# Kernel tuning notes

Hardware: AMD Instinct MI355X
Metric: run time of the kernel (lower is better)

## Reference

```python
import jax, jax.numpy as jnp
import numpy as np

HEAD_SIZE = 64
EPS_GN = 1e-5 * 8 * 8  # GroupNorm eps = 1e-5 * head_size_divisor**2


def rwkv7_scan(w_raw, q, k, v, a, b):
    """RWKV-7 'wind backstepping' linear recurrence.
    Inputs [B,T,H,N]. Per step (matching the CUDA kernel):
      decay = exp(-exp(w_raw)); sa = S @ a; S = S*decay + sa b^T + v k^T; y = S @ q
    State S is [B,H,N_value,N_key]."""
    decay = jnp.exp(-jnp.exp(w_raw))
    B, T, H, N = q.shape
    xs = tuple(jnp.moveaxis(t, 1, 0) for t in (decay, q, k, v, a, b))  # [T,B,H,N]
    S0 = jnp.zeros((B, H, N, N), q.dtype)

    def step(S, inp):
        d, qt, kt, vt, at, bt = inp
        sa = jnp.einsum('bhij,bhj->bhi', S, at)
        S = S * d[:, :, None, :] + sa[..., None] * bt[:, :, None, :] + vt[..., None] * kt[:, :, None, :]
        y = jnp.einsum('bhij,bhj->bhi', S, qt)
        return S, y

    _, ys = jax.lax.scan(step, S0, xs)
    return jnp.moveaxis(ys, 0, 1)  # [B,T,H,N]


def setup_inputs() -> dict:
    key = jax.random.key(0)
    B, T, C, H, N = 4, 960, 2048, 32, 64
    Dw, Da, Dv, Dg = 96, 96, 64, 256
    ks = iter(jax.random.split(key, 40))

    def nrm(shape, s=0.02):
        return jax.random.normal(next(ks), shape, jnp.float32) * s

    def uni(shape):
        return jax.random.uniform(next(ks), shape, jnp.float32)

    return dict(
        x=nrm((B, T, C), 1.0),
        v_first=nrm((B, T, C), 1.0),
        x_r=uni((1, 1, C)), x_w=uni((1, 1, C)), x_k=uni((1, 1, C)),
        x_v=uni((1, 1, C)), x_a=uni((1, 1, C)), x_g=uni((1, 1, C)),
        w0=jnp.linspace(-7.0, -2.0, C, dtype=jnp.float32).reshape(1, 1, C) + 0.5,
        w1=nrm((C, Dw)), w2=nrm((Dw, C)),
        a0=nrm((1, 1, C)), a1=nrm((C, Da)), a2=nrm((Da, C)),
        v0=jnp.ones((1, 1, C), jnp.float32), v1=nrm((C, Dv)), v2=nrm((Dv, C)),
        g1=nrm((C, Dg)), g2=nrm((Dg, C)),
        k_k=jnp.full((1, 1, C), 0.85, jnp.float32),
        k_a=jnp.ones((1, 1, C), jnp.float32),
        r_k=nrm((H, N)),
        Wr=nrm((C, C)), Wk=nrm((C, C)), Wv=nrm((C, C)), Wo=nrm((C, C)),
        ln_w=jnp.ones((C,), jnp.float32), ln_b=jnp.zeros((C,), jnp.float32),
    )


def reference(x, v_first, x_r, x_w, x_k, x_v, x_a, x_g,
              w0, w1, w2, a0, a1, a2, v0, v1, v2, g1, g2,
              k_k, k_a, r_k, Wr, Wk, Wv, Wo, ln_w, ln_b):
    B, T, C = x.shape
    H = C // HEAD_SIZE
    # time_shift: ZeroPad2d((0,0,1,-1)) == shift right by 1 along T with zero at t=0
    x_prev = jnp.pad(x, ((0, 0), (1, 0), (0, 0)))[:, :T]
    xx = x_prev - x
    xr = x + xx * x_r; xw = x + xx * x_w; xk = x + xx * x_k
    xv = x + xx * x_v; xa = x + xx * x_a; xg = x + xx * x_g

    r = xr @ Wr.T
    w = -jax.nn.softplus(-(w0 + jnp.tanh(xw @ w1) @ w2)) - 0.5
    k = xk @ Wk.T
    v = xv @ Wv.T
    # layer_id != 0: residual-value mixing with first layer's value
    v = v + (v_first - v) * jax.nn.sigmoid(v0 + (xv @ v1) @ v2)
    a = jax.nn.sigmoid(a0 + (xa @ a1) @ a2)
    g = jax.nn.sigmoid(xg @ g1) @ g2

    kk = (k * k_k).reshape(B, T, H, HEAD_SIZE)
    kk = kk / jnp.maximum(jnp.linalg.norm(kk, axis=-1, keepdims=True), 1e-12)  # F.normalize
    kk = kk.reshape(B, T, C)
    k = k * (1 + (a - 1) * k_a)

    hs = lambda t: t.reshape(B, T, H, HEAD_SIZE)
    y = rwkv7_scan(hs(w), hs(r), hs(k), hs(v), hs(-kk), hs(kk * a)).reshape(B, T, C)

    # GroupNorm(H groups over C)
    yg = y.reshape(B, T, H, HEAD_SIZE)
    mu = yg.mean(-1, keepdims=True)
    var = yg.var(-1, keepdims=True)
    y = ((yg - mu) / jnp.sqrt(var + EPS_GN)).reshape(B, T, C) * ln_w + ln_b

    y = y + ((hs(r) * hs(k) * r_k).sum(-1, keepdims=True) * hs(v)).reshape(B, T, C)
    return (y * g) @ Wo.T
```

## Files before the change

### kernel.cpp

```cpp
#include <hip/hip_runtime.h>
#include <stdint.h>

#define BDIM 4
#define TDIM 960
#define CDIM 2048
#define HDIM 32
#define NDIM 64
#define BT   (BDIM*TDIM)

typedef unsigned short u16;
typedef __attribute__((ext_vector_type(8))) short short8;
typedef __attribute__((ext_vector_type(4))) float f32x4;

__device__ __forceinline__ float b2f(u16 u){
  union{unsigned int i; float f;}x; x.i=((unsigned int)u)<<16; return x.f;
}
__device__ __forceinline__ u16 f2b(float f){
  union{float f; unsigned int i;}x; x.f=f;
  unsigned int r = x.i + 0x7fffu + ((x.i>>16)&1u);
  return (u16)(r>>16);
}
__device__ __forceinline__ unsigned pk2(float lo, float hi){
  return (unsigned)f2b(lo) | ((unsigned)f2b(hi)<<16);
}
__device__ __forceinline__ void unpack8(uint4 p, float* o){
  o[0]=b2f((u16)(p.x&0xffff)); o[1]=b2f((u16)(p.x>>16));
  o[2]=b2f((u16)(p.y&0xffff)); o[3]=b2f((u16)(p.y>>16));
  o[4]=b2f((u16)(p.z&0xffff)); o[5]=b2f((u16)(p.z>>16));
  o[6]=b2f((u16)(p.w&0xffff)); o[7]=b2f((u16)(p.w>>16));
}
__device__ __forceinline__ uint4 pack8(const float* o){
  uint4 p;
  p.x = pk2(o[0],o[1]);
  p.y = pk2(o[2],o[3]);
  p.z = pk2(o[4],o[5]);
  p.w = pk2(o[6],o[7]);
  return p;
}
__device__ __forceinline__ void ld8f(const float* p, float* o){
  float4 a = *(const float4*)p;
  float4 b = *(const float4*)(p+4);
  o[0]=a.x;o[1]=a.y;o[2]=a.z;o[3]=a.w;o[4]=b.x;o[5]=b.y;o[6]=b.z;o[7]=b.w;
}
__device__ __forceinline__ float sigm(float x){ return 1.f/(1.f+expf(-x)); }
__device__ __forceinline__ void stc(float* p, float v){ *p = v; }
__device__ __forceinline__ void stc(u16* p, float v){ *p = f2b(v); }

__device__ __forceinline__ float row_red16(float x){
  x += __int_as_float(__builtin_amdgcn_update_dpp(0, __float_as_int(x), 0xB1,  0xF, 0xF, true));
  x += __int_as_float(__builtin_amdgcn_update_dpp(0, __float_as_int(x), 0x4E,  0xF, 0xF, true));
  x += __int_as_float(__builtin_amdgcn_update_dpp(0, __float_as_int(x), 0x141, 0xF, 0xF, true));
  x += __int_as_float(__builtin_amdgcn_update_dpp(0, __float_as_int(x), 0x140, 0xF, 0xF, true));
  return x;
}

__global__ __launch_bounds__(256) void cvt_kernel(const float* src, u16* dst){
  size_t i = ((size_t)blockIdx.x*256 + threadIdx.x)*8;
  float v[8]; ld8f(src+i, v);
  *(uint4*)(dst+i) = pack8(v);
}

struct TJob { const float* src; u16* dst; int R, Cs, DR, DC; };
struct TJobs8 { TJob j[8]; };

__global__ __launch_bounds__(256) void transpose_pad_kernel(TJobs8 jobs){
  TJob jb = jobs.j[blockIdx.z];
  int idx = blockIdx.x*256 + threadIdx.x;
  int total = jb.DR*jb.DC;
  if (idx >= total) return;
  int i = idx / jb.DC, k = idx % jb.DC;
  float v = 0.f;
  if (i < jb.Cs && k < jb.R) v = jb.src[(size_t)k*jb.Cs + i];
  jb.dst[idx] = f2b(v);
}

__global__ __launch_bounds__(256) void mix_kernel(
  const float* x,
  const float* cr, const float* cw, const float* ck,
  const float* cv, const float* ca, const float* cg,
  u16* mr, u16* mw, u16* mk, u16* mv, u16* ma, u16* mg)
{
  size_t tid = (size_t)blockIdx.x*256 + threadIdx.x;
  size_t base = tid*8;
  int c = (int)(base % CDIM);
  int row = (int)(base / CDIM);
  int t = row % TDIM;
  float xc[8], xp[8], xx[8], cf[8], o[8];
  ld8f(x+base, xc);
  if (t > 0) {
    ld8f(x+base-CDIM, xp);
  } else {
    for(int j=0;j<8;j++) xp[j]=0.f;
  }
  #pragma unroll
  for(int j=0;j<8;j++) xx[j]=xp[j]-xc[j];
#define DOMIX(CP, OP) do { ld8f(CP+c, cf); \
  _Pragma("unroll") for(int j=0;j<8;j++) o[j]=xc[j]+xx[j]*cf[j]; \
  *(uint4*)(OP+base)=pack8(o); } while(0)
  DOMIX(cr, mr); DOMIX(cw, mw); DOMIX(ck, mk);
  DOMIX(cv, mv); DOMIX(ca, ma); DOMIX(cg, mg);
#undef DOMIX
}

struct GemmJob {
  const u16* A; const u16* Bt; void* C;
  int nbm, nbn, K, lda, ldb, ldc;
};
struct GemmJobs { GemmJob j[4]; };

template<typename TC>
__global__ __launch_bounds__(256, 2) void gemm_bt_kernel(GemmJobs jobs){
  GemmJob jb = jobs.j[blockIdx.z];
  int bm = blockIdx.x % jb.nbm;
  int bn = blockIdx.x / jb.nbm;
  if (bn >= jb.nbn) return;
  __shared__ __attribute__((aligned(16))) u16 As[128*64];
  __shared__ __attribute__((aligned(16))) u16 Bs[128*64];
  int tid = threadIdx.x;
  int wave = tid>>6, lane = tid&63;
  int wr = wave>>1, wc = wave&1;
  f32x4 acc[4][4];
  #pragma unroll
  for(int i=0;i<4;i++)
    #pragma unroll
    for(int j=0;j<4;j++) acc[i][j] = (f32x4){0.f,0.f,0.f,0.f};
  const int rA0 = bm*128;
  const int rB0 = bn*128;
  int srow = (lane>>3);
  int scol = (lane&7)*8;
  for (int k0=0; k0<jb.K; k0+=64){
    #pragma unroll
    for (int it=0; it<4; ++it){
      int rr = wave*32 + it*8;
      const u16* gA = jb.A + (size_t)(rA0 + rr + srow)*jb.lda + (k0 + scol);
      __builtin_amdgcn_global_load_lds((const __attribute__((address_space(1))) void*)gA,
          (__attribute__((address_space(3))) void*)&As[rr*64], 16, 0, 0);
      const u16* gB = jb.Bt + (size_t)(rB0 + rr + srow)*jb.ldb + (k0 + scol);
      __builtin_amdgcn_global_load_lds((const __attribute__((address_space(1))) void*)gB,
          (__attribute__((address_space(3))) void*)&Bs[rr*64], 16, 0, 0);
    }
    __syncthreads();
    #pragma unroll
    for (int kc=0; kc<2; ++kc){
      short8 af[4], bfr[4];
      int ko = kc*32 + (lane>>4)*8;
      #pragma unroll
      for (int mi=0; mi<4; ++mi)
        af[mi] = *(const short8*)&As[(wr*64 + mi*16 + (lane&15))*64 + ko];
      #pragma unroll
      for (int ni=0; ni<4; ++ni)
        bfr[ni] = *(const short8*)&Bs[(wc*64 + ni*16 + (lane&15))*64 + ko];
      #pragma unroll
      for (int mi=0; mi<4; ++mi)
        #pragma unroll
        for (int ni=0; ni<4; ++ni)
          acc[mi][ni] = __builtin_amdgcn_mfma_f32_16x16x32_bf16(af[mi], bfr[ni], acc[mi][ni], 0, 0, 0);
    }
    __syncthreads();
  }
  TC* C = (TC*)jb.C;
  int cn = (lane&15);
  int rq = (lane>>4)*4;
  #pragma unroll
  for (int mi=0; mi<4; ++mi){
    #pragma unroll
    for (int ni=0; ni<4; ++ni){
      int col = rB0 + wc*64 + ni*16 + cn;
      int row = rA0 + wr*64 + mi*16 + rq;
      #pragma unroll
      for (int e=0; e<4; ++e)
        stc(&C[(size_t)(row+e)*jb.ldc + col], acc[mi][ni][e]);
    }
  }
}

__global__ __launch_bounds__(256) void act_kernel(u16* hw, u16* hg){
  int idx = blockIdx.x*256 + threadIdx.x;
  if (blockIdx.z==0){ if (idx < BT*128) hw[idx] = f2b(tanhf(b2f(hw[idx]))); }
  else              { if (idx < BT*256) hg[idx] = f2b(sigm(b2f(hg[idx]))); }
}

__global__ __launch_bounds__(256) void post_kernel(
  const u16* rbuf, const u16* kbuf, const u16* vraw, const float* vfirst,
  const u16* wl, const u16* al, const u16* vl,
  const float* w0, const float* a0, const float* v0,
  const float* kkc, const float* kac,
  float* dout, uint4* qki, uint4* abi, u16* vs)
{
  int row = blockIdx.x, tid = threadIdx.x;
  int c = tid*8;
  size_t base = (size_t)row*CDIM + c;
  float qf[8], kf[8], vr[8], vf[8], wlf[8], alf[8], vlf[8], w0f[8], a0f[8], v0f[8], kkf[8], kaf[8];
  unpack8(*(const uint4*)(rbuf+base), qf);
  unpack8(*(const uint4*)(kbuf+base), kf);
  unpack8(*(const uint4*)(vraw+base), vr);
  ld8f(vfirst+base, vf);
  unpack8(*(const uint4*)(wl+base), wlf);
  unpack8(*(const uint4*)(al+base), alf);
  unpack8(*(const uint4*)(vl+base), vlf);
  ld8f(w0+c, w0f);
  ld8f(a0+c, a0f);
  ld8f(v0+c, v0f);
  ld8f(kkc+c, kkf);
  ld8f(kac+c, kaf);
  float dv[8], av[8], vv[8], kkr[8], kfin[8], asv[8], bsv[8];
  float ssq = 0.f;
  #pragma unroll
  for (int j=0;j<8;j++){
    float wv = -log1pf(expf(-(w0f[j]+wlf[j]))) - 0.5f;
    dv[j]  = expf(-expf(wv));
    av[j]  = sigm(a0f[j]+alf[j]);
    vv[j]  = vr[j] + (vf[j]-vr[j])*sigm(v0f[j]+vlf[j]);
    kkr[j] = kf[j]*kkf[j];
    ssq   += kkr[j]*kkr[j];
    kfin[j]= kf[j]*(1.f + (av[j]-1.f)*kaf[j]);
  }
  ssq += __shfl_xor(ssq,1); ssq += __shfl_xor(ssq,2); ssq += __shfl_xor(ssq,4);
  float inv = 1.f/fmaxf(sqrtf(ssq), 1e-12f);
  #pragma unroll
  for (int j=0;j<8;j++){ float kkn = kkr[j]*inv; asv[j] = -kkn; bsv[j] = kkn*av[j]; }
  *(float4*)(dout+base)   = make_float4(dv[0],dv[1],dv[2],dv[3]);
  *(float4*)(dout+base+4) = make_float4(dv[4],dv[5],dv[6],dv[7]);
  uint4* qke = (uint4*)((char*)qki + (size_t)row*8192 + (size_t)c*4);
  qke[0] = make_uint4(pk2(qf[0],qf[1]), pk2(kfin[0],kfin[1]), pk2(qf[2],qf[3]), pk2(kfin[2],kfin[3]));
  qke[1] = make_uint4(pk2(qf[4],qf[5]), pk2(kfin[4],kfin[5]), pk2(qf[6],qf[7]), pk2(kfin[6],kfin[7]));
  uint4* abe = (uint4*)((char*)abi + (size_t)row*8192 + (size_t)c*4);
  abe[0] = make_uint4(pk2(asv[0],asv[1]), pk2(bsv[0],bsv[1]), pk2(asv[2],asv[3]), pk2(bsv[2],bsv[3]));
  abe[1] = make_uint4(pk2(asv[4],asv[5]), pk2(bsv[4],bsv[5]), pk2(asv[6],asv[7]), pk2(bsv[6],bsv[7]));
  *(uint4*)(vs+base) = pack8(vv);
}

__global__ __launch_bounds__(256, 2) void scan_kernel(
  const float* __restrict__ decayp, const uint4* __restrict__ qki,
  const uint4* __restrict__ abi, const u16* __restrict__ vs,
  float* __restrict__ yb)
{
  int blk = blockIdx.x;
  int b    = blk >> 7;
  int h    = (blk >> 2) & 31;
  int qtr  = blk & 3;
  int tid  = threadIdx.x;
  int jg   = tid & 15;
  int ii   = tid >> 4;
  int row  = qtr*16 + ii;

  const char* dP = (const char*)decayp + (size_t)b*TDIM*8192 + h*256 + jg*16;
  const char* qP = (const char*)qki    + (size_t)b*TDIM*8192 + h*256 + jg*16;
  const char* aP = (const char*)abi    + (size_t)b*TDIM*8192 + h*256 + jg*16;
  const char* vP = (const char*)vs     + (size_t)b*TDIM*4096 + h*128 + row*2;

  float S0=0.f, S1=0.f, S2=0.f, S3=0.f;

  struct SR { f32x4 d; uint4 qk; uint4 ab; u16 v; };
  auto ld = [&](int t)->SR{
    SR r; size_t o = (size_t)t*8192;
    r.d  = *(const f32x4*)(dP + o);
    r.qk = *(const uint4*)(qP + o);
    r.ab = *(const uint4*)(aP + o);
    r.v  = *(const u16*)(vP + (size_t)t*4096);
    return r;
  };
  auto dostep = [&](const SR& r)->float{
    float a0=b2f((u16)(r.ab.x&0xffff)), a1=b2f((u16)(r.ab.x>>16));
    float a2=b2f((u16)(r.ab.z&0xffff)), a3=b2f((u16)(r.ab.z>>16));
    float sap = (S0*a0 + S1*a1) + (S2*a2 + S3*a3);
    sap = row_red16(sap);
    float c0=b2f((u16)(r.ab.y&0xffff)), c1=b2f((u16)(r.ab.y>>16));
    float c2=b2f((u16)(r.ab.w&0xffff)), c3=b2f((u16)(r.ab.w>>16));
    float k0=b2f((u16)(r.qk.y&0xffff)), k1=b2f((u16)(r.qk.y>>16));
    float k2=b2f((u16)(r.qk.w&0xffff)), k3=b2f((u16)(r.qk.w>>16));
    float vi=b2f(r.v);
    S0 = S0*r.d[0] + sap*c0 + vi*k0;
    S1 = S1*r.d[1] + sap*c1 + vi*k1;
    S2 = S2*r.d[2] + sap*c2 + vi*k2;
    S3 = S3*r.d[3] + sap*c3 + vi*k3;
    return (S0*b2f((u16)(r.qk.x&0xffff)) + S1*b2f((u16)(r.qk.x>>16)))
         + (S2*b2f((u16)(r.qk.z&0xffff)) + S3*b2f((u16)(r.qk.z>>16)));
  };

  SR A0=ld(0), A1=ld(1), A2=ld(2), A3=ld(3), A4=ld(4), A5=ld(5), A6=ld(6), A7=ld(7);
  for (int g=0; g<120; ++g){
    int tn = g*8 + 8;
    float yp[8];
#define STEPR(AR, S_) { yp[S_] = dostep(AR); int t_ = tn + (S_); \
    AR = ld(t_ < TDIM ? t_ : TDIM-1); }
    STEPR(A0,0) STEPR(A1,1) __builtin_amdgcn_sched_barrier(0);
    STEPR(A2,2) STEPR(A3,3) __builtin_amdgcn_sched_barrier(0);
    STEPR(A4,4) STEPR(A5,5) __builtin_amdgcn_sched_barrier(0);
    STEPR(A6,6) STEPR(A7,7) __builtin_amdgcn_sched_barrier(0);
#undef STEPR
    #pragma unroll
    for (int s=0; s<8; ++s) yp[s] = row_red16(yp[s]);
    if (jg < 8){
      float out = 0.f;
      #pragma unroll
      for (int s=0; s<8; ++s) if (jg==s) out = yp[s];
      yb[(size_t)b*TDIM*CDIM + (size_t)(g*8+jg)*CDIM + h*NDIM + row] = out;
    }
  }
}

__global__ __launch_bounds__(256) void final_kernel(
  const float* yb, const uint4* qki, const u16* vs,
  const float* rk, const float* lnw, const float* lnb, const u16* gl, u16* yg)
{
  int row = blockIdx.x, tid = threadIdx.x;
  int c = tid*8;
  size_t base = (size_t)row*CDIM + c;
  float y[8], rf[8], kf[8], vf[8], rkf[8], lw[8], lb[8], gf[8];
  ld8f(yb+base, y);
  const uint4* qke = (const uint4*)((const char*)qki + (size_t)row*8192 + (size_t)c*4);
  uint4 e0 = qke[0], e1 = qke[1];
  rf[0]=b2f((u16)(e0.x&0xffff)); rf[1]=b2f((u16)(e0.x>>16));
  rf[2]=b2f((u16)(e0.z&0xffff)); rf[3]=b2f((u16)(e0.z>>16));
  rf[4]=b2f((u16)(e1.x&0xffff)); rf[5]=b2f((u16)(e1.x>>16));
  rf[6]=b2f((u16)(e1.z&0xffff)); rf[7]=b2f((u16)(e1.z>>16));
  kf[0]=b2f((u16)(e0.y&0xffff)); kf[1]=b2f((u16)(e0.y>>16));
  kf[2]=b2f((u16)(e0.w&0xffff)); kf[3]=b2f((u16)(e0.w>>16));
  kf[4]=b2f((u16)(e1.y&0xffff)); kf[5]=b2f((u16)(e1.y>>16));
  kf[6]=b2f((u16)(e1.w&0xffff)); kf[7]=b2f((u16)(e1.w>>16));
  unpack8(*(const uint4*)(vs+base), vf);
  ld8f(rk+c,  rkf);
  ld8f(lnw+c, lw);
  ld8f(lnb+c, lb);
  unpack8(*(const uint4*)(gl+base), gf);
  float sy=0.f, syy=0.f, coef=0.f;
  #pragma unroll
  for (int j=0;j<8;j++){ sy+=y[j]; syy+=y[j]*y[j]; coef += rf[j]*kf[j]*rkf[j]; }
  sy  += __shfl_xor(sy,1);  sy  += __shfl_xor(sy,2);  sy  += __shfl_xor(sy,4);
  syy += __shfl_xor(syy,1); syy += __shfl_xor(syy,2); syy += __shfl_xor(syy,4);
  coef+= __shfl_xor(coef,1);coef+= __shfl_xor(coef,2);coef+= __shfl_xor(coef,4);
  float mu  = sy*(1.f/64.f);
  float var = syy*(1.f/64.f) - mu*mu;
  float rs  = rsqrtf(var + 6.4e-4f);
  float o[8];
  #pragma unroll
  for (int j=0;j<8;j++)
    o[j] = (((y[j]-mu)*rs)*lw[j] + lb[j] + coef*vf[j]) * gf[j];
  *(uint4*)(yg+base) = pack8(o);
}

extern "C" void kernel_launch(void* const* d_in, const int* in_sizes, int n_in,
                              void* d_out, int out_size, void* d_ws, size_t ws_size,
                              hipStream_t stream)
{
  const float* x      = (const float*)d_in[0];
  const float* vfirst = (const float*)d_in[1];
  const float* c_r = (const float*)d_in[2];
  const float* c_w = (const float*)d_in[3];
  const float* c_k = (const float*)d_in[4];
  const float* c_v = (const float*)d_in[5];
  const float* c_a = (const float*)d_in[6];
  const float* c_g = (const float*)d_in[7];
  const float* w0i = (const float*)d_in[8];
  const float* w1i = (const float*)d_in[9];
  const float* w2i = (const float*)d_in[10];
  const float* a0i = (const float*)d_in[11];
  const float* a1i = (const float*)d_in[12];
  const float* a2i = (const float*)d_in[13];
  const float* v0i = (const float*)d_in[14];
  const float* v1i = (const float*)d_in[15];
  const float* v2i = (const float*)d_in[16];
  const float* g1i = (const float*)d_in[17];
  const float* g2i = (const float*)d_in[18];
  const float* kki = (const float*)d_in[19];
  const float* kai = (const float*)d_in[20];
  const float* rki = (const float*)d_in[21];
  const float* Wr  = (const float*)d_in[22];
  const float* Wk  = (const float*)d_in[23];
  const float* Wv  = (const float*)d_in[24];
  const float* Wo  = (const float*)d_in[25];
  const float* lnw = (const float*)d_in[26];
  const float* lnb = (const float*)d_in[27];

  char* ws = (char*)d_ws;
  const size_t S2 = (size_t)BT*CDIM*2;
  u16* MIXR = (u16*)(ws + 0*S2);
  u16* MIXW = (u16*)(ws + 1*S2);
  u16* MIXK = (u16*)(ws + 2*S2);
  u16* MIXV = (u16*)(ws + 3*S2);
  u16* MIXA = (u16*)(ws + 4*S2);
  u16* MIXG = (u16*)(ws + 5*S2);
  u16* RBUF = (u16*)(ws + 6*S2);
  u16* KBUF = (u16*)(ws + 7*S2);
  u16* VRAW = (u16*)(ws + 8*S2);
  char* WB = ws + 9*S2;
  u16* WSLOT = (u16*)WB;
  char* WT = WB + 8388608;
  u16* W1T = (u16*)(WT + 0);
  u16* A1T = (u16*)(WT + 524288);
  u16* V1T = (u16*)(WT + 1048576);
  u16* G1T = (u16*)(WT + 1572864);
  u16* W2T = (u16*)(WT + 2621440);
  u16* A2T = (u16*)(WT + 3145728);
  u16* V2T = (u16*)(WT + 3670016);
  u16* G2T = (u16*)(WT + 4194304);
  char* HB = WT + 5242880;
  u16* HW = (u16*)(HB + 0);
  u16* HA = (u16*)(HB + 983040);
  u16* HV = (u16*)(HB + 1966080);
  u16* HG = (u16*)(HB + 2949120);
  char* L2 = HB + 4915200;
  u16* WL = (u16*)(L2 + 0*S2);
  u16* AL = (u16*)(L2 + 1*S2);
  u16* VL = (u16*)(L2 + 2*S2);
  u16* GL = (u16*)(L2 + 3*S2);
  float* WDEC = (float*)(ws + 0*S2);
  uint4* QKI  = (uint4*)(ws + 2*S2);
  uint4* ABI  = (uint4*)(ws + 4*S2);
  u16*   VS6  = (u16*)(ws + 6*S2);
  float* YBUF = (float*)(L2 + 0*S2);
  u16* YG = (u16*)(L2 + 2*S2);
  (void)in_sizes; (void)n_in; (void)out_size; (void)ws_size;

  TJobs8 tj;
  tj.j[0] = (TJob){w1i, W1T, 2048,  96, 128, 2048};
  tj.j[1] = (TJob){a1i, A1T, 2048,  96, 128, 2048};
  tj.j[2] = (TJob){v1i, V1T, 2048,  64, 128, 2048};
  tj.j[3] = (TJob){g1i, G1T, 2048, 256, 256, 2048};
  tj.j[4] = (TJob){w2i, W2T,   96, 2048, 2048, 128};
  tj.j[5] = (TJob){a2i, A2T,   96, 2048, 2048, 128};
  tj.j[6] = (TJob){v2i, V2T,   64, 2048, 2048, 128};
  tj.j[7] = (TJob){g2i, G2T,  256, 2048, 2048, 256};
  transpose_pad_kernel<<<dim3(2048,1,8), 256, 0, stream>>>(tj);

  mix_kernel<<<dim3(BT*CDIM/8/256), 256, 0, stream>>>(
      x, c_r, c_w, c_k, c_v, c_a, c_g, MIXR, MIXW, MIXK, MIXV, MIXA, MIXG);

  {
    GemmJobs gj;
    cvt_kernel<<<dim3(2048), 256, 0, stream>>>(Wr, WSLOT);
    gj.j[0] = (GemmJob){MIXR, WSLOT, RBUF, 30, 16, 2048, 2048, 2048, 2048};
    gj.j[1] = gj.j[0]; gj.j[2] = gj.j[0]; gj.j[3] = gj.j[0];
    gemm_bt_kernel<u16><<<dim3(480,1,1), 256, 0, stream>>>(gj);
    cvt_kernel<<<dim3(2048), 256, 0, stream>>>(Wk, WSLOT);
    gj.j[0] = (GemmJob){MIXK, WSLOT, KBUF, 30, 16, 2048, 2048, 2048, 2048};
    gemm_bt_kernel<u16><<<dim3(480,1,1), 256, 0, stream>>>(gj);
    cvt_kernel<<<dim3(2048), 256, 0, stream>>>(Wv, WSLOT);
    gj.j[0] = (GemmJob){MIXV, WSLOT, VRAW, 30, 16, 2048, 2048, 2048, 2048};
    gemm_bt_kernel<u16><<<dim3(480,1,1), 256, 0, stream>>>(gj);
  }

  GemmJobs lj1;
  lj1.j[0] = (GemmJob){MIXW, W1T, HW, 30, 1, 2048, 2048, 2048, 128};
  lj1.j[1] = (GemmJob){MIXA, A1T, HA, 30, 1, 2048, 2048, 2048, 128};
  lj1.j[2] = (GemmJob){MIXV, V1T, HV, 30, 1, 2048, 2048, 2048, 128};
  lj1.j[3] = (GemmJob){MIXG, G1T, HG, 30, 2, 2048, 2048, 2048, 256};
  gemm_bt_kernel<u16><<<dim3(60,1,4), 256, 0, stream>>>(lj1);

  act_kernel<<<dim3(3840,1,2), 256, 0, stream>>>(HW, HG);

  GemmJobs lj2;
  lj2.j[0] = (GemmJob){HW, W2T, WL, 30, 16, 128, 128, 128, 2048};
  lj2.j[1] = (GemmJob){HA, A2T, AL, 30, 16, 128, 128, 128, 2048};
  lj2.j[2] = (GemmJob){HV, V2T, VL, 30, 16, 128, 128, 128, 2048};
  lj2.j[3] = (GemmJob){HG, G2T, GL, 30, 16, 256, 256, 256, 2048};
  gemm_bt_kernel<u16><<<dim3(480,1,4), 256, 0, stream>>>(lj2);

  post_kernel<<<dim3(BT), 256, 0, stream>>>(
      RBUF, KBUF, VRAW, vfirst, WL, AL, VL, w0i, a0i, v0i, kki, kai,
      WDEC, QKI, ABI, VS6);

  scan_kernel<<<dim3(512), 256, 0, stream>>>(
      WDEC, QKI, ABI, VS6, YBUF);

  final_kernel<<<dim3(BT), 256, 0, stream>>>(
      YBUF, QKI, VS6, rki, lnw, lnb, GL, YG);

  cvt_kernel<<<dim3(2048), 256, 0, stream>>>(Wo, WSLOT);
  GemmJobs oj;
  oj.j[0] = (GemmJob){YG, WSLOT, d_out, 30, 16, 2048, 2048, 2048, 2048};
  oj.j[1] = oj.j[0]; oj.j[2] = oj.j[0]; oj.j[3] = oj.j[0];
  gemm_bt_kernel<float><<<dim3(480,1,1), 256, 0, stream>>>(oj);
}
```

Baseline: 823.3 us.

## Split scan state across 32 lanes per row with 1024 blocks

```diff
diff --git a/kernel.cpp b/kernel.cpp
--- a/kernel.cpp
+++ b/kernel.cpp
@@ -52,6 +52,9 @@
   x += __int_as_float(__builtin_amdgcn_update_dpp(0, __float_as_int(x), 0x141, 0xF, 0xF, true));
   x += __int_as_float(__builtin_amdgcn_update_dpp(0, __float_as_int(x), 0x140, 0xF, 0xF, true));
   return x;
+}
+__device__ __forceinline__ float xor16(float x){
+  return __int_as_float(__builtin_amdgcn_ds_swizzle(__float_as_int(x), 0x401F));
 }
 
 __global__ __launch_bounds__(256) void cvt_kernel(const float* src, u16* dst){
@@ -230,52 +233,47 @@
   *(uint4*)(vs+base) = pack8(vv);
 }
 
-__global__ __launch_bounds__(256, 2) void scan_kernel(
-  const float* __restrict__ decayp, const uint4* __restrict__ qki,
-  const uint4* __restrict__ abi, const u16* __restrict__ vs,
+__global__ __launch_bounds__(256, 4) void scan_kernel(
+  const float* __restrict__ decayp, const uint2* __restrict__ qki,
+  const uint2* __restrict__ abi, const u16* __restrict__ vs,
   float* __restrict__ yb)
 {
   int blk = blockIdx.x;
-  int b    = blk >> 7;
-  int h    = (blk >> 2) & 31;
-  int qtr  = blk & 3;
-  int tid  = threadIdx.x;
-  int jg   = tid & 15;
-  int ii   = tid >> 4;
-  int row  = qtr*16 + ii;
-
-  const char* dP = (const char*)decayp + (size_t)b*TDIM*8192 + h*256 + jg*16;
-  const char* qP = (const char*)qki    + (size_t)b*TDIM*8192 + h*256 + jg*16;
-  const char* aP = (const char*)abi    + (size_t)b*TDIM*8192 + h*256 + jg*16;
+  int b   = blk >> 8;
+  int h   = (blk >> 3) & 31;
+  int oct = blk & 7;
+  int tid = threadIdx.x;
+  int jg  = tid & 31;
+  int ii  = tid >> 5;
+  int row = oct*8 + ii;
+
+  const char* dP = (const char*)decayp + (size_t)b*TDIM*8192 + h*256 + jg*8;
+  const char* qP = (const char*)qki    + (size_t)b*TDIM*8192 + h*256 + jg*8;
+  const char* aP = (const char*)abi    + (size_t)b*TDIM*8192 + h*256 + jg*8;
   const char* vP = (const char*)vs     + (size_t)b*TDIM*4096 + h*128 + row*2;
 
-  float S0=0.f, S1=0.f, S2=0.f, S3=0.f;
-
-  struct SR { f32x4 d; uint4 qk; uint4 ab; u16 v; };
+  float Sx=0.f, Sy=0.f;
+
+  struct SR { float2 d; uint2 qk; uint2 ab; u16 v; };
   auto ld = [&](int t)->SR{
     SR r; size_t o = (size_t)t*8192;
-    r.d  = *(const f32x4*)(dP + o);
-    r.qk = *(const uint4*)(qP + o);
-    r.ab = *(const uint4*)(aP + o);
+    r.d  = *(const float2*)(dP + o);
+    r.qk = *(const uint2*)(qP + o);
+    r.ab = *(const uint2*)(aP + o);
     r.v  = *(const u16*)(vP + (size_t)t*4096);
     return r;
   };
   auto dostep = [&](const SR& r)->float{
-    float a0=b2f((u16)(r.ab.x&0xffff)), a1=b2f((u16)(r.ab.x>>16));
-    float a2=b2f((u16)(r.ab.z&0xffff)), a3=b2f((u16)(r.ab.z>>16));
-    float sap = (S0*a0 + S1*a1) + (S2*a2 + S3*a3);
+    float aLo=b2f((u16)(r.ab.x&0xffff)), aHi=b2f((u16)(r.ab.x>>16));
+    float sap = Sx*aLo + Sy*aHi;
     sap = row_red16(sap);
-    float c0=b2f((u16)(r.ab.y&0xffff)), c1=b2f((u16)(r.ab.y>>16));
-    float c2=b2f((u16)(r.ab.w&0xffff)), c3=b2f((u16)(r.ab.w>>16));
-    float k0=b2f((u16)(r.qk.y&0xffff)), k1=b2f((u16)(r.qk.y>>16));
-    float k2=b2f((u16)(r.qk.w&0xffff)), k3=b2f((u16)(r.qk.w>>16));
-    float vi=b2f(r.v);
-    S0 = S0*r.d[0] + sap*c0 + vi*k0;
-    S1 = S1*r.d[1] + sap*c1 + vi*k1;
-    S2 = S2*r.d[2] + sap*c2 + vi*k2;
-    S3 = S3*r.d[3] + sap*c3 + vi*k3;
-    return (S0*b2f((u16)(r.qk.x&0xffff)) + S1*b2f((u16)(r.qk.x>>16)))
-         + (S2*b2f((u16)(r.qk.z&0xffff)) + S3*b2f((u16)(r.qk.z>>16)));
+    sap += xor16(sap);
+    float bLo=b2f((u16)(r.ab.y&0xffff)), bHi=b2f((u16)(r.ab.y>>16));
+    float kLo=b2f((u16)(r.qk.y&0xffff)), kHi=b2f((u16)(r.qk.y>>16));
+    float vi =b2f(r.v);
+    Sx = Sx*r.d.x + sap*bLo + vi*kLo;
+    Sy = Sy*r.d.y + sap*bHi + vi*kHi;
+    return Sx*b2f((u16)(r.qk.x&0xffff)) + Sy*b2f((u16)(r.qk.x>>16));
   };
 
   SR A0=ld(0), A1=ld(1), A2=ld(2), A3=ld(3), A4=ld(4), A5=ld(5), A6=ld(6), A7=ld(7);
@@ -290,7 +288,10 @@
     STEPR(A6,6) STEPR(A7,7) __builtin_amdgcn_sched_barrier(0);
 #undef STEPR
     #pragma unroll
-    for (int s=0; s<8; ++s) yp[s] = row_red16(yp[s]);
+    for (int s=0; s<8; ++s){
+      yp[s] = row_red16(yp[s]);
+      yp[s] += xor16(yp[s]);
+    }
     if (jg < 8){
       float out = 0.f;
       #pragma unroll
@@ -461,8 +462,8 @@
       RBUF, KBUF, VRAW, vfirst, WL, AL, VL, w0i, a0i, v0i, kki, kai,
       WDEC, QKI, ABI, VS6);
 
-  scan_kernel<<<dim3(512), 256, 0, stream>>>(
-      WDEC, QKI, ABI, VS6, YBUF);
+  scan_kernel<<<dim3(1024), 256, 0, stream>>>(
+      WDEC, (const uint2*)QKI, (const uint2*)ABI, VS6, YBUF);
 
   final_kernel<<<dim3(BT), 256, 0, stream>>>(
       YBUF, QKI, VS6, rki, lnw, lnb, GL, YG);
```

New measurement: 986.8 us. +19.9%, slower.

## Store scan operands as fp32 planar arrays and precompute r·k coefficient in post

Applied to the files above, without the earlier changes.

```diff
diff --git a/kernel.cpp b/kernel.cpp
--- a/kernel.cpp
+++ b/kernel.cpp
@@ -11,6 +11,7 @@
 typedef unsigned short u16;
 typedef __attribute__((ext_vector_type(8))) short short8;
 typedef __attribute__((ext_vector_type(4))) float f32x4;
+typedef __attribute__((ext_vector_type(2))) float f32x2;
 
 __device__ __forceinline__ float b2f(u16 u){
   union{unsigned int i; float f;}x; x.i=((unsigned int)u)<<16; return x.f;
@@ -45,6 +46,8 @@
 __device__ __forceinline__ float sigm(float x){ return 1.f/(1.f+expf(-x)); }
 __device__ __forceinline__ void stc(float* p, float v){ *p = v; }
 __device__ __forceinline__ void stc(u16* p, float v){ *p = f2b(v); }
+__device__ __forceinline__ f32x2 lo2(f32x4 v){ return __builtin_shufflevector(v, v, 0, 1); }
+__device__ __forceinline__ f32x2 hi2(f32x4 v){ return __builtin_shufflevector(v, v, 2, 3); }
 
 __device__ __forceinline__ float row_red16(float x){
   x += __int_as_float(__builtin_amdgcn_update_dpp(0, __float_as_int(x), 0xB1,  0xF, 0xF, true));
@@ -184,13 +187,14 @@
   const u16* rbuf, const u16* kbuf, const u16* vraw, const float* vfirst,
   const u16* wl, const u16* al, const u16* vl,
   const float* w0, const float* a0, const float* v0,
-  const float* kkc, const float* kac,
-  float* dout, uint4* qki, uint4* abi, u16* vs)
+  const float* kkc, const float* kac, const float* rki,
+  float* dout, float* af, float* bf, float* kflo, float* kfhi,
+  u16* vs, float* coefp)
 {
   int row = blockIdx.x, tid = threadIdx.x;
   int c = tid*8;
   size_t base = (size_t)row*CDIM + c;
-  float qf[8], kf[8], vr[8], vf[8], wlf[8], alf[8], vlf[8], w0f[8], a0f[8], v0f[8], kkf[8], kaf[8];
+  float qf[8], kf[8], vr[8], vf[8], wlf[8], alf[8], vlf[8], w0f[8], a0f[8], v0f[8], kkf[8], kaf[8], rkf[8];
   unpack8(*(const uint4*)(rbuf+base), qf);
   unpack8(*(const uint4*)(kbuf+base), kf);
   unpack8(*(const uint4*)(vraw+base), vr);
@@ -203,6 +207,7 @@
   ld8f(v0+c, v0f);
   ld8f(kkc+c, kkf);
   ld8f(kac+c, kaf);
+  ld8f(rki+c, rkf);
   float dv[8], av[8], vv[8], kkr[8], kfin[8], asv[8], bsv[8];
   float ssq = 0.f;
   #pragma unroll
@@ -217,23 +222,35 @@
   }
   ssq += __shfl_xor(ssq,1); ssq += __shfl_xor(ssq,2); ssq += __shfl_xor(ssq,4);
   float inv = 1.f/fmaxf(sqrtf(ssq), 1e-12f);
-  #pragma unroll
-  for (int j=0;j<8;j++){ float kkn = kkr[j]*inv; asv[j] = -kkn; bsv[j] = kkn*av[j]; }
+  float coef = 0.f;
+  #pragma unroll
+  for (int j=0;j<8;j++){
+    float kkn = kkr[j]*inv; asv[j] = -kkn; bsv[j] = kkn*av[j];
+    coef += qf[j]*kfin[j]*rkf[j];
+  }
+  coef += __shfl_xor(coef,1); coef += __shfl_xor(coef,2); coef += __shfl_xor(coef,4);
+  __syncthreads();
   *(float4*)(dout+base)   = make_float4(dv[0],dv[1],dv[2],dv[3]);
   *(float4*)(dout+base+4) = make_float4(dv[4],dv[5],dv[6],dv[7]);
-  uint4* qke = (uint4*)((char*)qki + (size_t)row*8192 + (size_t)c*4);
-  qke[0] = make_uint4(pk2(qf[0],qf[1]), pk2(kfin[0],kfin[1]), pk2(qf[2],qf[3]), pk2(kfin[2],kfin[3]));
-  qke[1] = make_uint4(pk2(qf[4],qf[5]), pk2(kfin[4],kfin[5]), pk2(qf[6],qf[7]), pk2(kfin[6],kfin[7]));
-  uint4* abe = (uint4*)((char*)abi + (size_t)row*8192 + (size_t)c*4);
-  abe[0] = make_uint4(pk2(asv[0],asv[1]), pk2(bsv[0],bsv[1]), pk2(asv[2],asv[3]), pk2(bsv[2],bsv[3]));
-  abe[1] = make_uint4(pk2(asv[4],asv[5]), pk2(bsv[4],bsv[5]), pk2(asv[6],asv[7]), pk2(bsv[6],bsv[7]));
+  float* afp = af + base;
+  *(float4*)(afp)   = make_float4(asv[0],asv[1],asv[2],asv[3]);
+  *(float4*)(afp+4) = make_float4(asv[4],asv[5],asv[6],asv[7]);
+  float* bfp = bf + base;
+  *(float4*)(bfp)   = make_float4(bsv[0],bsv[1],bsv[2],bsv[3]);
+  *(float4*)(bfp+4) = make_float4(bsv[4],bsv[5],bsv[6],bsv[7]);
+  float* kfp = (c < 1024) ? (kflo + (size_t)row*1024 + c)
+                          : (kfhi + (size_t)row*1024 + (c-1024));
+  *(float4*)(kfp)   = make_float4(kfin[0],kfin[1],kfin[2],kfin[3]);
+  *(float4*)(kfp+4) = make_float4(kfin[4],kfin[5],kfin[6],kfin[7]);
   *(uint4*)(vs+base) = pack8(vv);
+  if ((tid&7)==0) coefp[(size_t)row*32 + (tid>>3)] = coef;
 }
 
 __global__ __launch_bounds__(256, 2) void scan_kernel(
-  const float* __restrict__ decayp, const uint4* __restrict__ qki,
-  const uint4* __restrict__ abi, const u16* __restrict__ vs,
-  float* __restrict__ yb)
+  const float* __restrict__ decayp, const u16* __restrict__ qb,
+  const float* __restrict__ kflo, const float* __restrict__ kfhi,
+  const float* __restrict__ af, const float* __restrict__ bf,
+  const u16* __restrict__ vs, float* __restrict__ yb)
 {
   int blk = blockIdx.x;
   int b    = blk >> 7;
@@ -244,38 +261,43 @@
   int ii   = tid >> 4;
   int row  = qtr*16 + ii;
 
-  const char* dP = (const char*)decayp + (size_t)b*TDIM*8192 + h*256 + jg*16;
-  const char* qP = (const char*)qki    + (size_t)b*TDIM*8192 + h*256 + jg*16;
-  const char* aP = (const char*)abi    + (size_t)b*TDIM*8192 + h*256 + jg*16;
-  const char* vP = (const char*)vs     + (size_t)b*TDIM*4096 + h*128 + row*2;
-
-  float S0=0.f, S1=0.f, S2=0.f, S3=0.f;
-
-  struct SR { f32x4 d; uint4 qk; uint4 ab; u16 v; };
+  size_t co4 = (size_t)(h*256 + jg*16);
+  const char* dP = (const char*)decayp + (size_t)b*TDIM*8192 + co4;
+  const char* aP = (const char*)af     + (size_t)b*TDIM*8192 + co4;
+  const char* bP = (const char*)bf     + (size_t)b*TDIM*8192 + co4;
+  const char* kP = (h < 16)
+      ? ((const char*)kflo + (size_t)b*TDIM*4096 + (size_t)(h*256 + jg*16))
+      : ((const char*)kfhi + (size_t)b*TDIM*4096 + (size_t)((h-16)*256 + jg*16));
+  const char* qP = (const char*)qb + (size_t)b*TDIM*4096 + (size_t)(h*128 + jg*8);
+  const char* vP = (const char*)vs + (size_t)b*TDIM*4096 + (size_t)(h*128 + row*2);
+
+  f32x2 Sa = (f32x2){0.f,0.f}, Sb = (f32x2){0.f,0.f};
+
+  struct SR { f32x4 d, k, a, b; uint2 q; u16 v; };
   auto ld = [&](int t)->SR{
-    SR r; size_t o = (size_t)t*8192;
-    r.d  = *(const f32x4*)(dP + o);
-    r.qk = *(const uint4*)(qP + o);
-    r.ab = *(const uint4*)(aP + o);
-    r.v  = *(const u16*)(vP + (size_t)t*4096);
+    SR r;
+    size_t o8 = (size_t)t*8192, o4 = (size_t)t*4096;
+    r.d = *(const f32x4*)(dP + o8);
+    r.a = *(const f32x4*)(aP + o8);
+    r.b = *(const f32x4*)(bP + o8);
+    r.k = *(const f32x4*)(kP + o4);
+    r.q = *(const uint2*)(qP + o4);
+    r.v = *(const u16*)(vP + o4);
     return r;
   };
   auto dostep = [&](const SR& r)->float{
-    float a0=b2f((u16)(r.ab.x&0xffff)), a1=b2f((u16)(r.ab.x>>16));
-    float a2=b2f((u16)(r.ab.z&0xffff)), a3=b2f((u16)(r.ab.z>>16));
-    float sap = (S0*a0 + S1*a1) + (S2*a2 + S3*a3);
+    f32x2 t = Sa*lo2(r.a) + Sb*hi2(r.a);
+    float sap = t[0] + t[1];
     sap = row_red16(sap);
-    float c0=b2f((u16)(r.ab.y&0xffff)), c1=b2f((u16)(r.ab.y>>16));
-    float c2=b2f((u16)(r.ab.w&0xffff)), c3=b2f((u16)(r.ab.w>>16));
-    float k0=b2f((u16)(r.qk.y&0xffff)), k1=b2f((u16)(r.qk.y>>16));
-    float k2=b2f((u16)(r.qk.w&0xffff)), k3=b2f((u16)(r.qk.w>>16));
-    float vi=b2f(r.v);
-    S0 = S0*r.d[0] + sap*c0 + vi*k0;
-    S1 = S1*r.d[1] + sap*c1 + vi*k1;
-    S2 = S2*r.d[2] + sap*c2 + vi*k2;
-    S3 = S3*r.d[3] + sap*c3 + vi*k3;
-    return (S0*b2f((u16)(r.qk.x&0xffff)) + S1*b2f((u16)(r.qk.x>>16)))
-         + (S2*b2f((u16)(r.qk.z&0xffff)) + S3*b2f((u16)(r.qk.z>>16)));
+    float vi = b2f(r.v);
+    f32x2 s2 = (f32x2){sap,sap};
+    f32x2 v2 = (f32x2){vi,vi};
+    Sa = Sa*lo2(r.d) + s2*lo2(r.b) + v2*lo2(r.k);
+    Sb = Sb*hi2(r.d) + s2*hi2(r.b) + v2*hi2(r.k);
+    f32x2 q01 = (f32x2){b2f((u16)(r.q.x&0xffff)), b2f((u16)(r.q.x>>16))};
+    f32x2 q23 = (f32x2){b2f((u16)(r.q.y&0xffff)), b2f((u16)(r.q.y>>16))};
+    f32x2 u = Sa*q01 + Sb*q23;
+    return u[0] + u[1];
   };
 
   SR A0=ld(0), A1=ld(1), A2=ld(2), A3=ld(3), A4=ld(4), A5=ld(5), A6=ld(6), A7=ld(7);
@@ -301,35 +323,24 @@
 }
 
 __global__ __launch_bounds__(256) void final_kernel(
-  const float* yb, const uint4* qki, const u16* vs,
-  const float* rk, const float* lnw, const float* lnb, const u16* gl, u16* yg)
+  const float* yb, const u16* vs, const float* coefp,
+  const float* lnw, const float* lnb, const u16* gl, u16* yg)
 {
   int row = blockIdx.x, tid = threadIdx.x;
   int c = tid*8;
   size_t base = (size_t)row*CDIM + c;
-  float y[8], rf[8], kf[8], vf[8], rkf[8], lw[8], lb[8], gf[8];
+  float y[8], vf[8], lw[8], lb[8], gf[8];
   ld8f(yb+base, y);
-  const uint4* qke = (const uint4*)((const char*)qki + (size_t)row*8192 + (size_t)c*4);
-  uint4 e0 = qke[0], e1 = qke[1];
-  rf[0]=b2f((u16)(e0.x&0xffff)); rf[1]=b2f((u16)(e0.x>>16));
-  rf[2]=b2f((u16)(e0.z&0xffff)); rf[3]=b2f((u16)(e0.z>>16));
-  rf[4]=b2f((u16)(e1.x&0xffff)); rf[5]=b2f((u16)(e1.x>>16));
-  rf[6]=b2f((u16)(e1.z&0xffff)); rf[7]=b2f((u16)(e1.z>>16));
-  kf[0]=b2f((u16)(e0.y&0xffff)); kf[1]=b2f((u16)(e0.y>>16));
-  kf[2]=b2f((u16)(e0.w&0xffff)); kf[3]=b2f((u16)(e0.w>>16));
-  kf[4]=b2f((u16)(e1.y&0xffff)); kf[5]=b2f((u16)(e1.y>>16));
-  kf[6]=b2f((u16)(e1.w&0xffff)); kf[7]=b2f((u16)(e1.w>>16));
   unpack8(*(const uint4*)(vs+base), vf);
-  ld8f(rk+c,  rkf);
   ld8f(lnw+c, lw);
   ld8f(lnb+c, lb);
   unpack8(*(const uint4*)(gl+base), gf);
-  float sy=0.f, syy=0.f, coef=0.f;
-  #pragma unroll
-  for (int j=0;j<8;j++){ sy+=y[j]; syy+=y[j]*y[j]; coef += rf[j]*kf[j]*rkf[j]; }
+  float coef = coefp[(size_t)row*32 + (tid>>3)];
+  float sy=0.f, syy=0.f;
+  #pragma unroll
+  for (int j=0;j<8;j++){ sy+=y[j]; syy+=y[j]*y[j]; }
   sy  += __shfl_xor(sy,1);  sy  += __shfl_xor(sy,2);  sy  += __shfl_xor(sy,4);
   syy += __shfl_xor(syy,1); syy += __shfl_xor(syy,2); syy += __shfl_xor(syy,4);
-  coef+= __shfl_xor(coef,1);coef+= __shfl_xor(coef,2);coef+= __shfl_xor(coef,4);
   float mu  = sy*(1.f/64.f);
   float var = syy*(1.f/64.f) - mu*mu;
   float rs  = rsqrtf(var + 6.4e-4f);
@@ -406,9 +417,12 @@
   u16* VL = (u16*)(L2 + 2*S2);
   u16* GL = (u16*)(L2 + 3*S2);
   float* WDEC = (float*)(ws + 0*S2);
-  uint4* QKI  = (uint4*)(ws + 2*S2);
-  uint4* ABI  = (uint4*)(ws + 4*S2);
-  u16*   VS6  = (u16*)(ws + 6*S2);
+  float* AF   = (float*)(ws + 2*S2);
+  float* BF   = (float*)(ws + 4*S2);
+  float* KFLO = (float*)(ws + 7*S2);
+  float* KFHI = (float*)(ws + 8*S2);
+  u16*   VSW  = (u16*)(WB);
+  float* COEF = (float*)(WB + 15728640);
   float* YBUF = (float*)(L2 + 0*S2);
   u16* YG = (u16*)(L2 + 2*S2);
   (void)in_sizes; (void)n_in; (void)out_size; (void)ws_size;
@@ -458,14 +472,14 @@
   gemm_bt_kernel<u16><<<dim3(480,1,4), 256, 0, stream>>>(lj2);
 
   post_kernel<<<dim3(BT), 256, 0, stream>>>(
-      RBUF, KBUF, VRAW, vfirst, WL, AL, VL, w0i, a0i, v0i, kki, kai,
-      WDEC, QKI, ABI, VS6);
+      RBUF, KBUF, VRAW, vfirst, WL, AL, VL, w0i, a0i, v0i, kki, kai, rki,
+      WDEC, AF, BF, KFLO, KFHI, VSW, COEF);
 
   scan_kernel<<<dim3(512), 256, 0, stream>>>(
-      WDEC, QKI, ABI, VS6, YBUF);
+      WDEC, RBUF, KFLO, KFHI, AF, BF, VSW, YBUF);
 
   final_kernel<<<dim3(BT), 256, 0, stream>>>(
-      YBUF, QKI, VS6, rki, lnw, lnb, GL, YG);
+      YBUF, VSW, COEF, lnw, lnb, GL, YG);
 
   cvt_kernel<<<dim3(2048), 256, 0, stream>>>(Wo, WSLOT);
   GemmJobs oj;
```

After: 901.8 us. +9.5%, slower.

## Batch R/K/V and LoRA-down GEMMs into one launch; vectorize scan state updates

Applied to the files above, without the earlier changes.

```diff
diff --git a/kernel.cpp b/kernel.cpp
--- a/kernel.cpp
+++ b/kernel.cpp
@@ -11,6 +11,7 @@
 typedef unsigned short u16;
 typedef __attribute__((ext_vector_type(8))) short short8;
 typedef __attribute__((ext_vector_type(4))) float f32x4;
+typedef __attribute__((ext_vector_type(2))) float f32x2;
 
 __device__ __forceinline__ float b2f(u16 u){
   union{unsigned int i; float f;}x; x.i=((unsigned int)u)<<16; return x.f;
@@ -45,6 +46,11 @@
 __device__ __forceinline__ float sigm(float x){ return 1.f/(1.f+expf(-x)); }
 __device__ __forceinline__ void stc(float* p, float v){ *p = v; }
 __device__ __forceinline__ void stc(u16* p, float v){ *p = f2b(v); }
+__device__ __forceinline__ f32x2 lo2(f32x4 v){ return __builtin_shufflevector(v, v, 0, 1); }
+__device__ __forceinline__ f32x2 hi2(f32x4 v){ return __builtin_shufflevector(v, v, 2, 3); }
+__device__ __forceinline__ f32x2 up2(unsigned w){
+  return (f32x2){ __int_as_float((int)(w<<16)), __int_as_float((int)(w & 0xffff0000u)) };
+}
 
 __device__ __forceinline__ float row_red16(float x){
   x += __int_as_float(__builtin_amdgcn_update_dpp(0, __float_as_int(x), 0xB1,  0xF, 0xF, true));
@@ -54,7 +60,10 @@
   return x;
 }
 
-__global__ __launch_bounds__(256) void cvt_kernel(const float* src, u16* dst){
+struct CvtJobs { const float* s[3]; u16* d[3]; };
+__global__ __launch_bounds__(256) void cvt_kernel(CvtJobs jobs){
+  const float* src = jobs.s[blockIdx.z];
+  u16* dst = jobs.d[blockIdx.z];
   size_t i = ((size_t)blockIdx.x*256 + threadIdx.x)*8;
   float v[8]; ld8f(src+i, v);
   *(uint4*)(dst+i) = pack8(v);
@@ -106,10 +115,10 @@
   const u16* A; const u16* Bt; void* C;
   int nbm, nbn, K, lda, ldb, ldc;
 };
-struct GemmJobs { GemmJob j[4]; };
+struct GemmJobs8 { GemmJob j[8]; };
 
 template<typename TC>
-__global__ __launch_bounds__(256, 2) void gemm_bt_kernel(GemmJobs jobs){
+__global__ __launch_bounds__(256, 2) void gemm_bt_kernel(GemmJobs8 jobs){
   GemmJob jb = jobs.j[blockIdx.z];
   int bm = blockIdx.x % jb.nbm;
   int bn = blockIdx.x / jb.nbm;
@@ -249,7 +258,7 @@
   const char* aP = (const char*)abi    + (size_t)b*TDIM*8192 + h*256 + jg*16;
   const char* vP = (const char*)vs     + (size_t)b*TDIM*4096 + h*128 + row*2;
 
-  float S0=0.f, S1=0.f, S2=0.f, S3=0.f;
+  f32x2 Sa = (f32x2){0.f,0.f}, Sb = (f32x2){0.f,0.f};
 
   struct SR { f32x4 d; uint4 qk; uint4 ab; u16 v; };
   auto ld = [&](int t)->SR{
@@ -261,21 +270,20 @@
     return r;
   };
   auto dostep = [&](const SR& r)->float{
-    float a0=b2f((u16)(r.ab.x&0xffff)), a1=b2f((u16)(r.ab.x>>16));
-    float a2=b2f((u16)(r.ab.z&0xffff)), a3=b2f((u16)(r.ab.z>>16));
-    float sap = (S0*a0 + S1*a1) + (S2*a2 + S3*a3);
+    f32x2 a01 = up2(r.ab.x), a23 = up2(r.ab.z);
+    f32x2 t = Sa*a01 + Sb*a23;
+    float sap = t[0] + t[1];
     sap = row_red16(sap);
-    float c0=b2f((u16)(r.ab.y&0xffff)), c1=b2f((u16)(r.ab.y>>16));
-    float c2=b2f((u16)(r.ab.w&0xffff)), c3=b2f((u16)(r.ab.w>>16));
-    float k0=b2f((u16)(r.qk.y&0xffff)), k1=b2f((u16)(r.qk.y>>16));
-    float k2=b2f((u16)(r.qk.w&0xffff)), k3=b2f((u16)(r.qk.w>>16));
-    float vi=b2f(r.v);
-    S0 = S0*r.d[0] + sap*c0 + vi*k0;
-    S1 = S1*r.d[1] + sap*c1 + vi*k1;
-    S2 = S2*r.d[2] + sap*c2 + vi*k2;
-    S3 = S3*r.d[3] + sap*c3 + vi*k3;
-    return (S0*b2f((u16)(r.qk.x&0xffff)) + S1*b2f((u16)(r.qk.x>>16)))
-         + (S2*b2f((u16)(r.qk.z&0xffff)) + S3*b2f((u16)(r.qk.z>>16)));
+    f32x2 b01 = up2(r.ab.y), b23 = up2(r.ab.w);
+    f32x2 k01 = up2(r.qk.y), k23 = up2(r.qk.w);
+    float vi = b2f(r.v);
+    f32x2 s2 = (f32x2){sap, sap};
+    f32x2 v2 = (f32x2){vi, vi};
+    Sa = Sa*lo2(r.d) + s2*b01 + v2*k01;
+    Sb = Sb*hi2(r.d) + s2*b23 + v2*k23;
+    f32x2 q01 = up2(r.qk.x), q23 = up2(r.qk.z);
+    f32x2 u = Sa*q01 + Sb*q23;
+    return u[0] + u[1];
   };
 
   SR A0=ld(0), A1=ld(1), A2=ld(2), A3=ld(3), A4=ld(4), A5=ld(5), A6=ld(6), A7=ld(7);
@@ -405,6 +413,8 @@
   u16* AL = (u16*)(L2 + 1*S2);
   u16* VL = (u16*)(L2 + 2*S2);
   u16* GL = (u16*)(L2 + 3*S2);
+  u16* WK2 = (u16*)(L2 + 0);
+  u16* WV2 = (u16*)(L2 + 8388608);
   float* WDEC = (float*)(ws + 0*S2);
   uint4* QKI  = (uint4*)(ws + 2*S2);
   uint4* ABI  = (uint4*)(ws + 4*S2);
@@ -427,34 +437,31 @@
   mix_kernel<<<dim3(BT*CDIM/8/256), 256, 0, stream>>>(
       x, c_r, c_w, c_k, c_v, c_a, c_g, MIXR, MIXW, MIXK, MIXV, MIXA, MIXG);
 
-  {
-    GemmJobs gj;
-    cvt_kernel<<<dim3(2048), 256, 0, stream>>>(Wr, WSLOT);
-    gj.j[0] = (GemmJob){MIXR, WSLOT, RBUF, 30, 16, 2048, 2048, 2048, 2048};
-    gj.j[1] = gj.j[0]; gj.j[2] = gj.j[0]; gj.j[3] = gj.j[0];
-    gemm_bt_kernel<u16><<<dim3(480,1,1), 256, 0, stream>>>(gj);
-    cvt_kernel<<<dim3(2048), 256, 0, stream>>>(Wk, WSLOT);
-    gj.j[0] = (GemmJob){MIXK, WSLOT, KBUF, 30, 16, 2048, 2048, 2048, 2048};
-    gemm_bt_kernel<u16><<<dim3(480,1,1), 256, 0, stream>>>(gj);
-    cvt_kernel<<<dim3(2048), 256, 0, stream>>>(Wv, WSLOT);
-    gj.j[0] = (GemmJob){MIXV, WSLOT, VRAW, 30, 16, 2048, 2048, 2048, 2048};
-    gemm_bt_kernel<u16><<<dim3(480,1,1), 256, 0, stream>>>(gj);
-  }
-
-  GemmJobs lj1;
-  lj1.j[0] = (GemmJob){MIXW, W1T, HW, 30, 1, 2048, 2048, 2048, 128};
-  lj1.j[1] = (GemmJob){MIXA, A1T, HA, 30, 1, 2048, 2048, 2048, 128};
-  lj1.j[2] = (GemmJob){MIXV, V1T, HV, 30, 1, 2048, 2048, 2048, 128};
-  lj1.j[3] = (GemmJob){MIXG, G1T, HG, 30, 2, 2048, 2048, 2048, 256};
-  gemm_bt_kernel<u16><<<dim3(60,1,4), 256, 0, stream>>>(lj1);
+  CvtJobs cj;
+  cj.s[0] = Wr; cj.d[0] = WSLOT;
+  cj.s[1] = Wk; cj.d[1] = WK2;
+  cj.s[2] = Wv; cj.d[2] = WV2;
+  cvt_kernel<<<dim3(2048,1,3), 256, 0, stream>>>(cj);
+
+  GemmJobs8 mj;
+  mj.j[0] = (GemmJob){MIXR, WSLOT, RBUF, 30, 16, 2048, 2048, 2048, 2048};
+  mj.j[1] = (GemmJob){MIXK, WK2,   KBUF, 30, 16, 2048, 2048, 2048, 2048};
+  mj.j[2] = (GemmJob){MIXV, WV2,   VRAW, 30, 16, 2048, 2048, 2048, 2048};
+  mj.j[3] = (GemmJob){MIXW, W1T, HW, 30, 1, 2048, 2048, 2048, 128};
+  mj.j[4] = (GemmJob){MIXA, A1T, HA, 30, 1, 2048, 2048, 2048, 128};
+  mj.j[5] = (GemmJob){MIXV, V1T, HV, 30, 1, 2048, 2048, 2048, 128};
+  mj.j[6] = (GemmJob){MIXG, G1T, HG, 30, 2, 2048, 2048, 2048, 256};
+  mj.j[7] = mj.j[0];
+  gemm_bt_kernel<u16><<<dim3(480,1,7), 256, 0, stream>>>(mj);
 
   act_kernel<<<dim3(3840,1,2), 256, 0, stream>>>(HW, HG);
 
-  GemmJobs lj2;
+  GemmJobs8 lj2;
   lj2.j[0] = (GemmJob){HW, W2T, WL, 30, 16, 128, 128, 128, 2048};
   lj2.j[1] = (GemmJob){HA, A2T, AL, 30, 16, 128, 128, 128, 2048};
   lj2.j[2] = (GemmJob){HV, V2T, VL, 30, 16, 128, 128, 128, 2048};
   lj2.j[3] = (GemmJob){HG, G2T, GL, 30, 16, 256, 256, 256, 2048};
+  lj2.j[4] = lj2.j[0]; lj2.j[5] = lj2.j[0]; lj2.j[6] = lj2.j[0]; lj2.j[7] = lj2.j[0];
   gemm_bt_kernel<u16><<<dim3(480,1,4), 256, 0, stream>>>(lj2);
 
   post_kernel<<<dim3(BT), 256, 0, stream>>>(
@@ -467,9 +474,13 @@
   final_kernel<<<dim3(BT), 256, 0, stream>>>(
       YBUF, QKI, VS6, rki, lnw, lnb, GL, YG);
 
-  cvt_kernel<<<dim3(2048), 256, 0, stream>>>(Wo, WSLOT);
-  GemmJobs oj;
+  CvtJobs co;
+  co.s[0] = Wo; co.d[0] = WSLOT;
+  co.s[1] = Wo; co.d[1] = WSLOT;
+  co.s[2] = Wo; co.d[2] = WSLOT;
+  cvt_kernel<<<dim3(2048,1,1), 256, 0, stream>>>(co);
+  GemmJobs8 oj;
   oj.j[0] = (GemmJob){YG, WSLOT, d_out, 30, 16, 2048, 2048, 2048, 2048};
-  oj.j[1] = oj.j[0]; oj.j[2] = oj.j[0]; oj.j[3] = oj.j[0];
+  for (int i=1;i<8;i++) oj.j[i] = oj.j[0];
   gemm_bt_kernel<float><<<dim3(480,1,1), 256, 0, stream>>>(oj);
 }
```

Measured after the change: 726.9 us. 1.13x faster.
